# Optimization experiments

Hardware: AMD Instinct MI355X
Metric: run time of the kernel (lower is better)

Reference implementation:

```python
import jax, jax.numpy as jnp
import numpy as np

LN_EPS = 1e-5

def setup_inputs() -> dict:
    key = jax.random.key(0)
    ks = jax.random.split(key, 12)
    B, S, D = 4, 2048, 1024
    s = 1.0 / np.sqrt(D)
    return {
        "query": jax.random.normal(ks[0], (B, S, D), jnp.float32),
        "key_in": jax.random.normal(ks[1], (B, S, D), jnp.float32),
        "value": jax.random.normal(ks[2], (B, S, D), jnp.float32),
        "Wq": jax.random.normal(ks[3], (D, D), jnp.float32) * s,
        "bq": jax.random.normal(ks[4], (D,), jnp.float32) * s,
        "Wk": jax.random.normal(ks[5], (D, D), jnp.float32) * s,
        "bk": jax.random.normal(ks[6], (D,), jnp.float32) * s,
        "Wv": jax.random.normal(ks[7], (D, D), jnp.float32) * s,
        "bv": jax.random.normal(ks[8], (D,), jnp.float32) * s,
        "gamma": jnp.ones((D,), jnp.float32),
        "beta": jnp.zeros((D,), jnp.float32),
    }

def reference(query, key_in, value, Wq, bq, Wk, bk, Wv, bv, gamma, beta):
    # Linear projections (torch Linear: x @ W^T + b; here W stored as [in,out])
    q = jnp.einsum('bsd,df->bsf', query, Wq) + bq
    k = jnp.einsum('bsd,df->bsf', key_in, Wk) + bk
    v = jnp.einsum('bsd,df->bsf', value, Wv) + bv
    # Attention: note NO 1/sqrt(d) scaling, single head (faithful to source)
    attn = jnp.einsum('bqd,bkd->bqk', q, k)          # [B,S,S]
    probs = jax.nn.softmax(attn, axis=-1)
    result = jnp.einsum('bqk,bkd->bqd', probs, v)     # [B,S,D]
    # Residual + LayerNorm
    x = result + query
    mu = jnp.mean(x, axis=-1, keepdims=True)
    var = jnp.mean((x - mu) ** 2, axis=-1, keepdims=True)
    return (x - mu) * jax.lax.rsqrt(var + LN_EPS) * gamma + beta
```

## Files before the change

kernel.cpp:

```cpp
#include <hip/hip_runtime.h>
#include <hip/hip_bf16.h>
#include <cstdint>


typedef unsigned short u16;
typedef unsigned int   u32;
typedef _Float16 f16;
typedef f16   f16x8  __attribute__((ext_vector_type(8)));
typedef f16   f16x4  __attribute__((ext_vector_type(4)));
typedef float f32x4  __attribute__((ext_vector_type(4)));

#define DEV __device__ __forceinline__

DEV void gld_lds16(const f16* g, char* l){
  __builtin_amdgcn_global_load_lds(
      (const __attribute__((address_space(1))) u32*)(uintptr_t)g,
      (__attribute__((address_space(3))) u32*)(u32)(uintptr_t)l, 16, 0, 0);
}

DEV int swz_lid(){
  int lid = (blockIdx.z * gridDim.y + blockIdx.y) * gridDim.x + blockIdx.x;
  int cpx = (gridDim.x * gridDim.y * gridDim.z) >> 3;
  return (lid & 7) * cpx + (lid >> 3);
}

#define MFMA_(av, bv, ci, cj) \
  acc[ci][cj] = __builtin_amdgcn_mfma_f32_16x16x32_f16(av, bv, acc[ci][cj], 0, 0, 0)

template<bool MORE>
DEV void ktile32(const f16* (&src)[4], char* bufc, char* stash,
                 int ob0, int ob1, int aoffs, int boffs, f32x4 (&acc)[8][4])
{
  if (MORE){
    gld_lds16(src[0], stash +         ob0); src[0] += 32;
    gld_lds16(src[1], stash +         ob1); src[1] += 32;
    gld_lds16(src[2], stash + 16384 + ob0); src[2] += 32;
    gld_lds16(src[3], stash + 16384 + ob1); src[3] += 32;
    asm volatile("s_waitcnt vmcnt(4)\ns_barrier" ::: "memory");
  } else {
    asm volatile("s_waitcnt vmcnt(0)\ns_barrier" ::: "memory");
  }
  f16x8 a[8], b[4];
#pragma unroll
  for (int i = 0; i < 8; i++) a[i] = *(const f16x8*)(bufc + aoffs + i * 2048);
#pragma unroll
  for (int j = 0; j < 4; j++) b[j] = *(const f16x8*)(bufc + 16384 + boffs + j * 4096);
  __builtin_amdgcn_s_setprio(1);
#pragma unroll
  for (int i = 0; i < 8; i++)
#pragma unroll
    for (int j = 0; j < 4; j++) MFMA_(a[i], b[j], i, j);
  __builtin_amdgcn_s_setprio(0);
  __builtin_amdgcn_sched_barrier(0);
  __builtin_amdgcn_s_barrier();
}

DEV void gemm_core(const f16* __restrict__ A, int lda,
                   const f16* __restrict__ B, size_t ldb,
                   int nt, char* smem, f32x4 (&acc)[8][4])
{
  const int tid  = threadIdx.x;
  const int lane = tid & 63;
  const int wv   = tid >> 6;
  const int wm   = wv >> 2, wn = wv & 3;
  const int lr   = lane & 15, lq = lane >> 4;

  const int o0 = tid * 16, o1 = o0 + 8192;
  const int r0 = o0 >> 6,  r1 = o1 >> 6;
  const int sl0 = ((o0 >> 4) & 3) ^ ((r0 >> 1) & 3);
  const int sl1 = ((o1 >> 4) & 3) ^ ((r1 >> 1) & 3);
  const f16* src[4];
  src[0] = A + (size_t)r0 * lda + sl0 * 8;
  src[1] = A + (size_t)r1 * lda + sl1 * 8;
  src[2] = B + (size_t)r0 * ldb + sl0 * 8;
  src[3] = B + (size_t)r1 * ldb + sl1 * 8;

  const int sw    = (lr >> 1) & 3;
  const int aoffs = (wm * 16 + lr) * 64 + ((lq ^ sw) << 4);
  const int boffs = (wn * 16 + lr) * 64 + ((lq ^ sw) << 4);

#pragma unroll
  for (int i = 0; i < 8; i++)
#pragma unroll
    for (int j = 0; j < 4; j++) acc[i][j] = (f32x4){0.f, 0.f, 0.f, 0.f};

  gld_lds16(src[0], smem +         o0); src[0] += 32;
  gld_lds16(src[1], smem +         o1); src[1] += 32;
  gld_lds16(src[2], smem + 16384 + o0); src[2] += 32;
  gld_lds16(src[3], smem + 16384 + o1); src[3] += 32;

  for (int t = 0; t < nt - 1; ++t){
    char* bufc  = smem + ((t & 1) << 15);
    char* stash = smem + (((t & 1) ^ 1) << 15);
    ktile32<true>(src, bufc, stash, o0, o1, aoffs, boffs, acc);
  }
  {
    char* bufc  = smem + (((nt - 1) & 1) << 15);
    char* stash = smem + ((((nt - 1) & 1) ^ 1) << 15);
    ktile32<false>(src, bufc, stash, o0, o1, aoffs, boffs, acc);
  }
}

__global__ __launch_bounds__(512, 2) void proj8p(
    const f16* __restrict__ xq, const f16* __restrict__ xk, const f16* __restrict__ xv,
    const f16* __restrict__ wq, const f16* __restrict__ wk, const f16* __restrict__ wv,
    const float* __restrict__ bq, const float* __restrict__ bk, const float* __restrict__ bv,
    f16* __restrict__ oq, f16* __restrict__ ok, f16* __restrict__ ovT)
{
  __shared__ char smem[65536];
  const int s  = swz_lid();
  const int bx = s & 3, by = (s >> 2) & 31, z = s >> 7;
  const int m0 = by * 256, n0 = bx * 256;
  const f16* A = (z == 0 ? xq : z == 1 ? xk : xv) + (size_t)m0 * 1024;
  const f16* B = (z == 0 ? wq : z == 1 ? wk : wv) + (size_t)n0 * 1024;
  const float* bias = (z == 0 ? bq : z == 1 ? bk : bv);

  f32x4 acc[8][4];
  gemm_core(A, 1024, B, 1024, 32, smem, acc);

  const int lane = threadIdx.x & 63;
  const int wv_  = threadIdx.x >> 6;
  const int wm = wv_ >> 2, wn = wv_ & 3;
  const int lr = lane & 15, rj = (lane >> 4) * 4;

  if (z < 2){
    f16* o = z ? ok : oq;
#pragma unroll
    for (int i = 0; i < 8; i++)
#pragma unroll
      for (int j = 0; j < 4; j++){
        int row = m0 + i * 32 + wm * 16 + rj;
        int col = n0 + j * 64 + wn * 16 + lr;
        float bvl = bias[col];
#pragma unroll
        for (int r = 0; r < 4; r++)
          o[(size_t)(row + r) * 1024 + col] = (f16)(acc[i][j][r] + bvl);
      }
  } else {
#pragma unroll
    for (int i = 0; i < 8; i++)
#pragma unroll
      for (int j = 0; j < 4; j++){
        int row = m0 + i * 32 + wm * 16 + rj;
        int col = n0 + j * 64 + wn * 16 + lr;
        float bvl = bias[col];
        f16x4 tv;
#pragma unroll
        for (int r = 0; r < 4; r++) tv[r] = (f16)(acc[i][j][r] + bvl);
        *(f16x4*)(ovT + (size_t)col * 8192 + row) = tv;
      }
  }
}

__global__ __launch_bounds__(512, 2) void qk8p(
    const f16* __restrict__ q, const f16* __restrict__ k, float* __restrict__ Sout)
{
  __shared__ char smem[65536];
  const int s  = swz_lid();
  const int bx = s & 7, by = (s >> 3) & 7, z = s >> 6;
  const int m0 = by * 256, n0 = bx * 256;
  const f16* A = q + (size_t)z * 2048 * 1024 + (size_t)m0 * 1024;
  const f16* B = k + (size_t)z * 2048 * 1024 + (size_t)n0 * 1024;

  f32x4 acc[8][4];
  gemm_core(A, 1024, B, 1024, 32, smem, acc);

  const int lane = threadIdx.x & 63;
  const int wv_  = threadIdx.x >> 6;
  const int wm = wv_ >> 2, wn = wv_ & 3;
  const int lr = lane & 15, rj = (lane >> 4) * 4;
  float* o = Sout + (size_t)z * 2048 * 2048;
#pragma unroll
  for (int i = 0; i < 8; i++)
#pragma unroll
    for (int j = 0; j < 4; j++){
      int row = m0 + i * 32 + wm * 16 + rj;
      int col = n0 + j * 64 + wn * 16 + lr;
#pragma unroll
      for (int r = 0; r < 4; r++)
        o[(size_t)(row + r) * 2048 + col] = acc[i][j][r];
    }
}

__global__ __launch_bounds__(512, 2) void pv8p(
    const f16* __restrict__ P, const f16* __restrict__ vT, f16* __restrict__ O)
{
  __shared__ char smem[65536];
  const int s  = swz_lid();
  const int bx = s & 3, by = (s >> 2) & 7, z = s >> 5;
  const int zb = z >> 2, h = z & 3;
  const int m0 = by * 256, n0 = bx * 256;
  const f16* A = P  + (size_t)zb * 2048 * 2048 + (size_t)m0 * 2048 + h * 512;
  const f16* B = vT + (size_t)n0 * 8192 + (size_t)zb * 2048 + h * 512;

  f32x4 acc[8][4];
  gemm_core(A, 2048, B, 8192, 16, smem, acc);

  const int lane = threadIdx.x & 63;
  const int wv_  = threadIdx.x >> 6;
  const int wm = wv_ >> 2, wn = wv_ & 3;
  const int lr = lane & 15, rj = (lane >> 4) * 4;
  f16* o = O + (size_t)h * 8388608 + (size_t)zb * 2048 * 1024;
#pragma unroll
  for (int i = 0; i < 8; i++)
#pragma unroll
    for (int j = 0; j < 4; j++){
      int row = m0 + i * 32 + wm * 16 + rj;
      int col = n0 + j * 64 + wn * 16 + lr;
#pragma unroll
      for (int r = 0; r < 4; r++)
        o[(size_t)(row + r) * 1024 + col] = (f16)acc[i][j][r];
    }
}

__global__ __launch_bounds__(256) void cvt3_f32_f16(
    const float* __restrict__ x0, const float* __restrict__ x1, const float* __restrict__ x2,
    f16* __restrict__ y0, f16* __restrict__ y1, f16* __restrict__ y2){
  const int z = blockIdx.y;
  const float* x = z == 0 ? x0 : z == 1 ? x1 : x2;
  f16* y = z == 0 ? y0 : z == 1 ? y1 : y2;
  int i = (blockIdx.x * 256 + threadIdx.x) * 8;
  float4 a = *(const float4*)(x + i);
  float4 b = *(const float4*)(x + i + 4);
  f16x8 v;
  v[0]=(f16)a.x; v[1]=(f16)a.y; v[2]=(f16)a.z; v[3]=(f16)a.w;
  v[4]=(f16)b.x; v[5]=(f16)b.y; v[6]=(f16)b.z; v[7]=(f16)b.w;
  *(f16x8*)(y + i) = v;
}

__global__ __launch_bounds__(256) void transpose3_cvt_w(
    const float* __restrict__ W0, const float* __restrict__ W1, const float* __restrict__ W2,
    f16* __restrict__ T0, f16* __restrict__ T1, f16* __restrict__ T2, int D){
  const int z = blockIdx.z;
  const float* W = z == 0 ? W0 : z == 1 ? W1 : W2;
  f16* T = z == 0 ? T0 : z == 1 ? T1 : T2;
  __shared__ float t[32][33];
  int tx = threadIdx.x & 31, ty = threadIdx.x >> 5;
  int bx = blockIdx.x * 32, by = blockIdx.y * 32;
#pragma unroll
  for (int j = 0; j < 4; j++) t[ty + j*8][tx] = W[(size_t)(by + ty + j*8) * D + bx + tx];
  __syncthreads();
#pragma unroll
  for (int j = 0; j < 4; j++){
    float v = t[tx][ty + j*8];
    T[(size_t)(bx + ty + j*8) * D + by + tx] = (f16)v;
  }
}

__global__ __launch_bounds__(256) void softmax_rows(const float* __restrict__ S, f16* __restrict__ P){
  const int row  = blockIdx.x * 4 + (threadIdx.x >> 6);
  const int lane = threadIdx.x & 63;
  const float* x = S + (size_t)row * 2048 + lane * 32;
  float v[32];
  float m = -3.4e38f;
#pragma unroll
  for (int c = 0; c < 8; c++){
    float4 t = *(const float4*)(x + c * 4);
    v[c*4+0] = t.x; v[c*4+1] = t.y; v[c*4+2] = t.z; v[c*4+3] = t.w;
    m = fmaxf(m, fmaxf(fmaxf(t.x, t.y), fmaxf(t.z, t.w)));
  }
#pragma unroll
  for (int o = 32; o; o >>= 1) m = fmaxf(m, __shfl_xor(m, o));
  float ssum = 0.f;
#pragma unroll
  for (int j = 0; j < 32; j++){ v[j] = __expf(v[j] - m); ssum += v[j]; }
#pragma unroll
  for (int o = 32; o; o >>= 1) ssum += __shfl_xor(ssum, o);
  float inv = 1.f / ssum;
  f16* p = P + (size_t)row * 2048 + lane * 32;
#pragma unroll
  for (int c = 0; c < 4; c++){
    f16x8 ov;
#pragma unroll
    for (int j = 0; j < 8; j++) ov[j] = (f16)(v[c*8+j] * inv);
    *(f16x8*)(p + c * 8) = ov;
  }
}

DEV float wred_sum(float v){
#pragma unroll
  for (int o = 32; o; o >>= 1) v += __shfl_xor(v, o);
  return v;
}

__global__ __launch_bounds__(256) void resid_ln4(const f16* __restrict__ O,
                                                 const float* __restrict__ query,
                                                 const float* __restrict__ gamma,
                                                 const float* __restrict__ beta,
                                                 float* __restrict__ out){
  const int row = blockIdx.x;
  const int tid = threadIdx.x;
  const size_t base = (size_t)row * 1024 + tid * 4;
  float4 q4 = *(const float4*)(query + base);
  float x[4] = {q4.x, q4.y, q4.z, q4.w};
#pragma unroll
  for (int h = 0; h < 4; h++){
    f16x4 o4 = *(const f16x4*)(O + (size_t)h * 8388608 + base);
#pragma unroll
    for (int j = 0; j < 4; j++) x[j] += (float)o4[j];
  }
  float s = 0.f, ss = 0.f;
#pragma unroll
  for (int j = 0; j < 4; j++){ s += x[j]; ss += x[j] * x[j]; }

  __shared__ float red[4];
  s = wred_sum(s);
  if ((tid & 63) == 0) red[tid >> 6] = s;
  __syncthreads();
  s = red[0] + red[1] + red[2] + red[3];
  ss = wred_sum(ss);
  __syncthreads();
  if ((tid & 63) == 0) red[tid >> 6] = ss;
  __syncthreads();
  ss = red[0] + red[1] + red[2] + red[3];

  float mu = s * (1.f / 1024.f);
  float var = ss * (1.f / 1024.f) - mu * mu;
  float rs = rsqrtf(var + 1e-5f);
  float4 g4 = *(const float4*)(gamma + tid * 4);
  float4 b4 = *(const float4*)(beta + tid * 4);
  float4 r;
  r.x = (x[0] - mu) * rs * g4.x + b4.x;
  r.y = (x[1] - mu) * rs * g4.y + b4.y;
  r.z = (x[2] - mu) * rs * g4.z + b4.z;
  r.w = (x[3] - mu) * rs * g4.w + b4.w;
  *(float4*)(out + base) = r;
}

extern "C" void kernel_launch(void* const* d_in, const int* in_sizes, int n_in,
                              void* d_out, int out_size, void* d_ws, size_t ws_size,
                              hipStream_t stream){
  const float* query  = (const float*)d_in[0];
  const float* key_in = (const float*)d_in[1];
  const float* value  = (const float*)d_in[2];
  const float* Wq = (const float*)d_in[3];
  const float* bq = (const float*)d_in[4];
  const float* Wk = (const float*)d_in[5];
  const float* bk = (const float*)d_in[6];
  const float* Wv = (const float*)d_in[7];
  const float* bv = (const float*)d_in[8];
  const float* gamma = (const float*)d_in[9];
  const float* beta  = (const float*)d_in[10];

  const int B = 4, S = 2048, D = 1024;
  const int M = B * S;
  const size_t MB = 1ull << 20;
  char* ws = (char*)d_ws;

  f16* qf16 = (f16*)(ws + 0);
  f16* kf16 = (f16*)(ws + 16 * MB);
  f16* vT   = (f16*)(ws + 32 * MB);
  f16* wt_q = (f16*)(ws + 48 * MB);
  f16* wt_k = (f16*)(ws + 50 * MB);
  f16* wt_v = (f16*)(ws + 52 * MB);
  f16* Obuf = (f16*)(ws + 54 * MB);
  f16* xq   = (f16*)(ws + 118 * MB);
  f16* xk   = (f16*)(ws + 134 * MB);
  f16* xv   = (f16*)(ws + 150 * MB);
  float* Sbuf = (float*)(ws + 118 * MB);
  f16*   Pbuf = (f16*)(ws + 182 * MB);

  dim3 blk(256);
  const int nElem = M * D;

  cvt3_f32_f16<<<dim3(nElem / 2048, 3), blk, 0, stream>>>(query, key_in, value, xq, xk, xv);
  transpose3_cvt_w<<<dim3(32, 32, 3), blk, 0, stream>>>(Wq, Wk, Wv, wt_q, wt_k, wt_v, D);

  proj8p<<<dim3(4, 32, 3), dim3(512), 0, stream>>>(xq, xk, xv, wt_q, wt_k, wt_v,
                                                   bq, bk, bv, qf16, kf16, vT);

  qk8p<<<dim3(8, 8, 4), dim3(512), 0, stream>>>(qf16, kf16, Sbuf);

  softmax_rows<<<M / 4, blk, 0, stream>>>(Sbuf, Pbuf);

  pv8p<<<dim3(4, 8, 16), dim3(512), 0, stream>>>(Pbuf, vT, Obuf);

  resid_ln4<<<M, blk, 0, stream>>>(Obuf, query, gamma, beta, (float*)d_out);
}
```

Baseline: 228.1 us.

## Shrink GEMM block tiles to 128x256 and halve PV split-K factor

The shared GEMM core changes from 256x256 to 128x256 block tiles, with a 64x64 warp sub-tile, three async LDS loads per k-step, and 48KB of shared memory. This allows four blocks per CU and doubles the grid sizes for the projection, QK and PV kernels. The PV split-K drops from 4 to 2 partial outputs, so the residual LayerNorm reads two partial sums instead of four. The goal is better occupancy and less partial-sum traffic, at the cost of lower per-block arithmetic intensity and more global loads per FLOP.

```diff
diff --git a/kernel.cpp b/kernel.cpp
--- a/kernel.cpp
+++ b/kernel.cpp
@@ -28,26 +28,25 @@
   acc[ci][cj] = __builtin_amdgcn_mfma_f32_16x16x32_f16(av, bv, acc[ci][cj], 0, 0, 0)
 
 template<bool MORE>
-DEV void ktile32(const f16* (&src)[4], char* bufc, char* stash,
-                 int ob0, int ob1, int aoffs, int boffs, f32x4 (&acc)[8][4])
+DEV void ktile(const f16* (&src)[3], char* bufc, char* stash,
+               int o, int aoff, int boff, f32x4 (&acc)[4][4])
 {
   if (MORE){
-    gld_lds16(src[0], stash +         ob0); src[0] += 32;
-    gld_lds16(src[1], stash +         ob1); src[1] += 32;
-    gld_lds16(src[2], stash + 16384 + ob0); src[2] += 32;
-    gld_lds16(src[3], stash + 16384 + ob1); src[3] += 32;
-    asm volatile("s_waitcnt vmcnt(4)\ns_barrier" ::: "memory");
+    gld_lds16(src[0], stash +         o); src[0] += 32;
+    gld_lds16(src[1], stash +  8192 + o); src[1] += 32;
+    gld_lds16(src[2], stash + 16384 + o); src[2] += 32;
+    asm volatile("s_waitcnt vmcnt(3)\ns_barrier" ::: "memory");
   } else {
     asm volatile("s_waitcnt vmcnt(0)\ns_barrier" ::: "memory");
   }
-  f16x8 a[8], b[4];
-#pragma unroll
-  for (int i = 0; i < 8; i++) a[i] = *(const f16x8*)(bufc + aoffs + i * 2048);
-#pragma unroll
-  for (int j = 0; j < 4; j++) b[j] = *(const f16x8*)(bufc + 16384 + boffs + j * 4096);
+  f16x8 a[4], b[4];
+#pragma unroll
+  for (int i = 0; i < 4; i++) a[i] = *(const f16x8*)(bufc + aoff + i * 1024);
+#pragma unroll
+  for (int j = 0; j < 4; j++) b[j] = *(const f16x8*)(bufc + boff + j * 1024);
   __builtin_amdgcn_s_setprio(1);
 #pragma unroll
-  for (int i = 0; i < 8; i++)
+  for (int i = 0; i < 4; i++)
 #pragma unroll
     for (int j = 0; j < 4; j++) MFMA_(a[i], b[j], i, j);
   __builtin_amdgcn_s_setprio(0);
@@ -57,7 +56,7 @@
 
 DEV void gemm_core(const f16* __restrict__ A, int lda,
                    const f16* __restrict__ B, size_t ldb,
-                   int nt, char* smem, f32x4 (&acc)[8][4])
+                   int nt, char* smem, f32x4 (&acc)[4][4])
 {
   const int tid  = threadIdx.x;
   const int lane = tid & 63;
@@ -65,57 +64,54 @@
   const int wm   = wv >> 2, wn = wv & 3;
   const int lr   = lane & 15, lq = lane >> 4;
 
-  const int o0 = tid * 16, o1 = o0 + 8192;
-  const int r0 = o0 >> 6,  r1 = o1 >> 6;
-  const int sl0 = ((o0 >> 4) & 3) ^ ((r0 >> 1) & 3);
-  const int sl1 = ((o1 >> 4) & 3) ^ ((r1 >> 1) & 3);
-  const f16* src[4];
-  src[0] = A + (size_t)r0 * lda + sl0 * 8;
-  src[1] = A + (size_t)r1 * lda + sl1 * 8;
-  src[2] = B + (size_t)r0 * ldb + sl0 * 8;
-  src[3] = B + (size_t)r1 * ldb + sl1 * 8;
-
-  const int sw    = (lr >> 1) & 3;
-  const int aoffs = (wm * 16 + lr) * 64 + ((lq ^ sw) << 4);
-  const int boffs = (wn * 16 + lr) * 64 + ((lq ^ sw) << 4);
-
-#pragma unroll
-  for (int i = 0; i < 8; i++)
+  const int o  = tid * 16;
+  const int r0 = o >> 6;
+  const int sl = ((o >> 4) & 3) ^ ((r0 >> 1) & 3);
+  const f16* src[3];
+  src[0] = A + (size_t)r0 * lda + sl * 8;
+  src[1] = B + (size_t)r0 * ldb + sl * 8;
+  src[2] = B + (size_t)(128 + r0) * ldb + sl * 8;
+
+  const int sw   = (lr >> 1) & 3;
+  const int aoff =        (wm * 64 + lr) * 64 + ((lq ^ sw) << 4);
+  const int boff = 8192 + (wn * 64 + lr) * 64 + ((lq ^ sw) << 4);
+
+#pragma unroll
+  for (int i = 0; i < 4; i++)
 #pragma unroll
     for (int j = 0; j < 4; j++) acc[i][j] = (f32x4){0.f, 0.f, 0.f, 0.f};
 
-  gld_lds16(src[0], smem +         o0); src[0] += 32;
-  gld_lds16(src[1], smem +         o1); src[1] += 32;
-  gld_lds16(src[2], smem + 16384 + o0); src[2] += 32;
-  gld_lds16(src[3], smem + 16384 + o1); src[3] += 32;
+  gld_lds16(src[0], smem +         o); src[0] += 32;
+  gld_lds16(src[1], smem +  8192 + o); src[1] += 32;
+  gld_lds16(src[2], smem + 16384 + o); src[2] += 32;
 
   for (int t = 0; t < nt - 1; ++t){
-    char* bufc  = smem + ((t & 1) << 15);
-    char* stash = smem + (((t & 1) ^ 1) << 15);
-    ktile32<true>(src, bufc, stash, o0, o1, aoffs, boffs, acc);
+    char* bufc  = smem + (t & 1) * 24576;
+    char* stash = smem + ((t & 1) ^ 1) * 24576;
+    ktile<true>(src, bufc, stash, o, aoff, boff, acc);
   }
   {
-    char* bufc  = smem + (((nt - 1) & 1) << 15);
-    char* stash = smem + ((((nt - 1) & 1) ^ 1) << 15);
-    ktile32<false>(src, bufc, stash, o0, o1, aoffs, boffs, acc);
-  }
-}
-
-__global__ __launch_bounds__(512, 2) void proj8p(
+    char* bufc  = smem + ((nt - 1) & 1) * 24576;
+    char* stash = smem + (((nt - 1) & 1) ^ 1) * 24576;
+    ktile<false>(src, bufc, stash, o, aoff, boff, acc);
+  }
+}
+
+__global__ __launch_bounds__(512, 4) void proj8p(
     const f16* __restrict__ xq, const f16* __restrict__ xk, const f16* __restrict__ xv,
     const f16* __restrict__ wq, const f16* __restrict__ wk, const f16* __restrict__ wv,
     const float* __restrict__ bq, const float* __restrict__ bk, const float* __restrict__ bv,
     f16* __restrict__ oq, f16* __restrict__ ok, f16* __restrict__ ovT)
 {
-  __shared__ char smem[65536];
+  __shared__ char smem[49152];
   const int s  = swz_lid();
-  const int bx = s & 3, by = (s >> 2) & 31, z = s >> 7;
-  const int m0 = by * 256, n0 = bx * 256;
+  const int bx = s & 3, by = (s >> 2) & 63, z = s >> 8;
+  const int m0 = by * 128, n0 = bx * 256;
   const f16* A = (z == 0 ? xq : z == 1 ? xk : xv) + (size_t)m0 * 1024;
   const f16* B = (z == 0 ? wq : z == 1 ? wk : wv) + (size_t)n0 * 1024;
   const float* bias = (z == 0 ? bq : z == 1 ? bk : bv);
 
-  f32x4 acc[8][4];
+  f32x4 acc[4][4];
   gemm_core(A, 1024, B, 1024, 32, smem, acc);
 
   const int lane = threadIdx.x & 63;
@@ -126,11 +122,11 @@
   if (z < 2){
     f16* o = z ? ok : oq;
 #pragma unroll
-    for (int i = 0; i < 8; i++)
+    for (int i = 0; i < 4; i++)
 #pragma unroll
       for (int j = 0; j < 4; j++){
-        int row = m0 + i * 32 + wm * 16 + rj;
-        int col = n0 + j * 64 + wn * 16 + lr;
+        int row = m0 + wm * 64 + i * 16 + rj;
+        int col = n0 + wn * 64 + j * 16 + lr;
         float bvl = bias[col];
 #pragma unroll
         for (int r = 0; r < 4; r++)
@@ -138,11 +134,11 @@
       }
   } else {
 #pragma unroll
-    for (int i = 0; i < 8; i++)
+    for (int i = 0; i < 4; i++)
 #pragma unroll
       for (int j = 0; j < 4; j++){
-        int row = m0 + i * 32 + wm * 16 + rj;
-        int col = n0 + j * 64 + wn * 16 + lr;
+        int row = m0 + wm * 64 + i * 16 + rj;
+        int col = n0 + wn * 64 + j * 16 + lr;
         float bvl = bias[col];
         f16x4 tv;
 #pragma unroll
@@ -152,17 +148,17 @@
   }
 }
 
-__global__ __launch_bounds__(512, 2) void qk8p(
+__global__ __launch_bounds__(512, 4) void qk8p(
     const f16* __restrict__ q, const f16* __restrict__ k, float* __restrict__ Sout)
 {
-  __shared__ char smem[65536];
+  __shared__ char smem[49152];
   const int s  = swz_lid();
-  const int bx = s & 7, by = (s >> 3) & 7, z = s >> 6;
-  const int m0 = by * 256, n0 = bx * 256;
+  const int bx = s & 7, by = (s >> 3) & 15, z = s >> 7;
+  const int m0 = by * 128, n0 = bx * 256;
   const f16* A = q + (size_t)z * 2048 * 1024 + (size_t)m0 * 1024;
   const f16* B = k + (size_t)z * 2048 * 1024 + (size_t)n0 * 1024;
 
-  f32x4 acc[8][4];
+  f32x4 acc[4][4];
   gemm_core(A, 1024, B, 1024, 32, smem, acc);
 
   const int lane = threadIdx.x & 63;
@@ -171,30 +167,30 @@
   const int lr = lane & 15, rj = (lane >> 4) * 4;
   float* o = Sout + (size_t)z * 2048 * 2048;
 #pragma unroll
-  for (int i = 0; i < 8; i++)
+  for (int i = 0; i < 4; i++)
 #pragma unroll
     for (int j = 0; j < 4; j++){
-      int row = m0 + i * 32 + wm * 16 + rj;
-      int col = n0 + j * 64 + wn * 16 + lr;
+      int row = m0 + wm * 64 + i * 16 + rj;
+      int col = n0 + wn * 64 + j * 16 + lr;
 #pragma unroll
       for (int r = 0; r < 4; r++)
         o[(size_t)(row + r) * 2048 + col] = acc[i][j][r];
     }
 }
 
-__global__ __launch_bounds__(512, 2) void pv8p(
+__global__ __launch_bounds__(512, 4) void pv8p(
     const f16* __restrict__ P, const f16* __restrict__ vT, f16* __restrict__ O)
 {
-  __shared__ char smem[65536];
+  __shared__ char smem[49152];
   const int s  = swz_lid();
-  const int bx = s & 3, by = (s >> 2) & 7, z = s >> 5;
-  const int zb = z >> 2, h = z & 3;
-  const int m0 = by * 256, n0 = bx * 256;
-  const f16* A = P  + (size_t)zb * 2048 * 2048 + (size_t)m0 * 2048 + h * 512;
-  const f16* B = vT + (size_t)n0 * 8192 + (size_t)zb * 2048 + h * 512;
-
-  f32x4 acc[8][4];
-  gemm_core(A, 2048, B, 8192, 16, smem, acc);
+  const int bx = s & 3, by = (s >> 2) & 15, z = s >> 6;
+  const int zb = z >> 1, h = z & 1;
+  const int m0 = by * 128, n0 = bx * 256;
+  const f16* A = P  + (size_t)zb * 2048 * 2048 + (size_t)m0 * 2048 + h * 1024;
+  const f16* B = vT + (size_t)n0 * 8192 + (size_t)zb * 2048 + h * 1024;
+
+  f32x4 acc[4][4];
+  gemm_core(A, 2048, B, 8192, 32, smem, acc);
 
   const int lane = threadIdx.x & 63;
   const int wv_  = threadIdx.x >> 6;
@@ -202,11 +198,11 @@
   const int lr = lane & 15, rj = (lane >> 4) * 4;
   f16* o = O + (size_t)h * 8388608 + (size_t)zb * 2048 * 1024;
 #pragma unroll
-  for (int i = 0; i < 8; i++)
+  for (int i = 0; i < 4; i++)
 #pragma unroll
     for (int j = 0; j < 4; j++){
-      int row = m0 + i * 32 + wm * 16 + rj;
-      int col = n0 + j * 64 + wn * 16 + lr;
+      int row = m0 + wm * 64 + i * 16 + rj;
+      int col = n0 + wn * 64 + j * 16 + lr;
 #pragma unroll
       for (int r = 0; r < 4; r++)
         o[(size_t)(row + r) * 1024 + col] = (f16)acc[i][j][r];
@@ -283,7 +279,8 @@
   return v;
 }
 
-__global__ __launch_bounds__(256) void resid_ln4(const f16* __restrict__ O,
+__global__ __launch_bounds__(256) void resid_ln2(const f16* __restrict__ O0,
+                                                 const f16* __restrict__ O1,
                                                  const float* __restrict__ query,
                                                  const float* __restrict__ gamma,
                                                  const float* __restrict__ beta,
@@ -291,14 +288,13 @@
   const int row = blockIdx.x;
   const int tid = threadIdx.x;
   const size_t base = (size_t)row * 1024 + tid * 4;
+  f16x4 o4 = *(const f16x4*)(O0 + base);
+  f16x4 p4 = *(const f16x4*)(O1 + base);
   float4 q4 = *(const float4*)(query + base);
-  float x[4] = {q4.x, q4.y, q4.z, q4.w};
-#pragma unroll
-  for (int h = 0; h < 4; h++){
-    f16x4 o4 = *(const f16x4*)(O + (size_t)h * 8388608 + base);
-#pragma unroll
-    for (int j = 0; j < 4; j++) x[j] += (float)o4[j];
-  }
+  float x[4] = {(float)o4[0] + (float)p4[0] + q4.x,
+                (float)o4[1] + (float)p4[1] + q4.y,
+                (float)o4[2] + (float)p4[2] + q4.z,
+                (float)o4[3] + (float)p4[3] + q4.w};
   float s = 0.f, ss = 0.f;
 #pragma unroll
   for (int j = 0; j < 4; j++){ s += x[j]; ss += x[j] * x[j]; }
@@ -366,14 +362,14 @@
   cvt3_f32_f16<<<dim3(nElem / 2048, 3), blk, 0, stream>>>(query, key_in, value, xq, xk, xv);
   transpose3_cvt_w<<<dim3(32, 32, 3), blk, 0, stream>>>(Wq, Wk, Wv, wt_q, wt_k, wt_v, D);
 
-  proj8p<<<dim3(4, 32, 3), dim3(512), 0, stream>>>(xq, xk, xv, wt_q, wt_k, wt_v,
+  proj8p<<<dim3(4, 64, 3), dim3(512), 0, stream>>>(xq, xk, xv, wt_q, wt_k, wt_v,
                                                    bq, bk, bv, qf16, kf16, vT);
 
-  qk8p<<<dim3(8, 8, 4), dim3(512), 0, stream>>>(qf16, kf16, Sbuf);
+  qk8p<<<dim3(8, 16, 4), dim3(512), 0, stream>>>(qf16, kf16, Sbuf);
 
   softmax_rows<<<M / 4, blk, 0, stream>>>(Sbuf, Pbuf);
 
-  pv8p<<<dim3(4, 8, 16), dim3(512), 0, stream>>>(Pbuf, vT, Obuf);
-
-  resid_ln4<<<M, blk, 0, stream>>>(Obuf, query, gamma, beta, (float*)d_out);
-}
+  pv8p<<<dim3(4, 16, 8), dim3(512), 0, stream>>>(Pbuf, vT, Obuf);
+
+  resid_ln2<<<M, blk, 0, stream>>>(Obuf, Obuf + 8388608, query, gamma, beta, (float*)d_out);
+}
```

Result: faster. 203.6 us (-10.8%).
